# Kernel optimization log

Measured on AMD Instinct MI355X. Metric: run time of the kernel, lower is better.

## Reference

```python
import jax, jax.numpy as jnp
import numpy as np

N_EMBD = 1024
HEAD_SIZE = 128
B, T = 8, 2048


def apply_rope(x):
    # x: (B, T, D); rotate interleaved pairs, matching torch view(B,T,D//2,2)
    b, t, d = x.shape
    freqs = 1.0 / (10000.0 ** (jnp.arange(0, d, 2, dtype=jnp.float32) / d))  # (D//2,)
    angles = jnp.arange(t, dtype=jnp.float32)[:, None] * freqs[None, :]      # (T, D//2)
    cos_a = jnp.cos(angles).astype(x.dtype)
    sin_a = jnp.sin(angles).astype(x.dtype)
    xr = x.reshape(b, t, d // 2, 2)
    x0, x1 = xr[..., 0], xr[..., 1]
    rot = jnp.stack([x0 * cos_a - x1 * sin_a, x0 * sin_a + x1 * cos_a], axis=-1)
    return rot.reshape(b, t, d)


def setup_inputs() -> dict:
    key = jax.random.key(0)
    kx, kq, kk, kv = jax.random.split(key, 4)
    x = jax.random.normal(kx, (B, T, N_EMBD), dtype=jnp.float32)
    scale = 0.02
    Wq = jax.random.normal(kq, (N_EMBD, HEAD_SIZE), dtype=jnp.float32) * scale
    Wk = jax.random.normal(kk, (N_EMBD, HEAD_SIZE), dtype=jnp.float32) * scale
    Wv = jax.random.normal(kv, (N_EMBD, HEAD_SIZE), dtype=jnp.float32) * scale
    return {"x": x, "Wq": Wq, "Wk": Wk, "Wv": Wv}


def reference(x, Wq, Wk, Wv):
    # QKV projections (bias=False)
    q = x @ Wq  # (B, T, H)
    k = x @ Wk
    v = x @ Wv
    q = apply_rope(q)
    k = apply_rope(k)
    d = k.shape[-1]
    wei = jnp.einsum('bqd,bkd->bqk', q, k) * (d ** -0.5)  # (B, T, T)
    causal = jnp.tril(jnp.ones((q.shape[1], q.shape[1]), dtype=bool))
    wei = jnp.where(causal, wei, jnp.finfo(wei.dtype).min)
    wei = jax.nn.softmax(wei, axis=-1)
    out = jnp.einsum('bqk,bkd->bqd', wei, v)  # (B, T, H)
    return out
```

## Files before the change

kernel.cpp:

```cpp
#include <hip/hip_runtime.h>
#include <math.h>

#define BB 8
#define TT 2048
#define EE 1024
#define DD 128

typedef _Float16 f16x8 __attribute__((ext_vector_type(8)));
typedef _Float16 f16x4 __attribute__((ext_vector_type(4)));
typedef float    f32x4 __attribute__((ext_vector_type(4)));
typedef float    f32x16 __attribute__((ext_vector_type(16)));

#define QSCALE 0.12752406f


__global__ __launch_bounds__(256)
void wt_prep_kernel(const float* __restrict__ Wq,
                    const float* __restrict__ Wk,
                    const float* __restrict__ Wv,
                    _Float16* __restrict__ Wb)
{
    int gid = blockIdx.x * 256 + threadIdx.x;
    int kc  = gid / 768;
    int rem = gid - kc * 768;
    int ns  = rem >> 6;
    int ln  = rem & 63;
    int n   = ns * 32 + (ln & 31);
    int k0  = kc * 16 + (ln >> 5) * 8;
    const float* __restrict__ W = (n < 128) ? Wq : (n < 256) ? Wk : Wv;
    int nl = n & 127;
    f16x8 w;
#pragma unroll
    for (int j = 0; j < 8; j++)
        w[j] = (_Float16)W[(size_t)(k0 + j) * DD + nl];
    *(f16x8*)&Wb[(size_t)gid * 8] = w;
}

__global__ __launch_bounds__(256)
void proj_rope_kernel(const float* __restrict__ x,
                      const _Float16* __restrict__ Wb,
                      _Float16* __restrict__ Qb,
                      _Float16* __restrict__ Ka,
                      _Float16* __restrict__ Va)
{
    const int r0   = blockIdx.x * 32;
    const int tid  = threadIdx.x;
    const int wave = tid >> 6;
    const int lane = tid & 63;
    const int half = lane >> 5;
    const int col  = lane & 31;

    __shared__ _Float16 Xb[2][2048];
    __shared__ _Float16 Out[32][136];

    f32x16 acc[3];
#pragma unroll
    for (int s = 0; s < 3; s++) acc[s] = (f32x16)0.f;

    const int sr = tid >> 3;
    const int sc = (tid & 7) * 4;
    const float* __restrict__ xp = &x[(size_t)(r0 + sr) * EE + sc];
    const int w0 = ((sc        >> 4) << 9) + ((sr + 32 * ((sc        >> 3) & 1)) << 3) + (sc & 7);
    const int w1 = (((sc + 32) >> 4) << 9) + ((sr + 32 * (((sc + 32) >> 3) & 1)) << 3) + (sc & 7);

    float4 pa0 = *(const float4*)(xp);
    float4 pa1 = *(const float4*)(xp + 32);
    {
        f16x4 h0 = { (_Float16)pa0.x, (_Float16)pa0.y, (_Float16)pa0.z, (_Float16)pa0.w };
        f16x4 h1 = { (_Float16)pa1.x, (_Float16)pa1.y, (_Float16)pa1.z, (_Float16)pa1.w };
        *(f16x4*)&Xb[0][w0] = h0;
        *(f16x4*)&Xb[0][w1] = h1;
    }
    float4 na0 = *(const float4*)(xp + 64);
    float4 na1 = *(const float4*)(xp + 96);
    float4 nb0 = *(const float4*)(xp + 128);
    float4 nb1 = *(const float4*)(xp + 160);

    for (int it = 0; it < 16; it++) {
        const int buf = it & 1;
        __syncthreads();
        f16x8 a[4], b[12];
#pragma unroll
        for (int kc = 0; kc < 4; kc++)
            a[kc] = *(f16x8*)&Xb[buf][(kc << 9) + lane * 8];
#pragma unroll
        for (int kc = 0; kc < 4; kc++)
#pragma unroll
            for (int s = 0; s < 3; s++)
                b[kc * 3 + s] = *(const f16x8*)&Wb[((size_t)(it * 4 + kc) * 12 + wave * 3 + s) * 512 + lane * 8];
#pragma unroll
        for (int kc = 0; kc < 4; kc++)
#pragma unroll
            for (int s = 0; s < 3; s++)
                acc[s] = __builtin_amdgcn_mfma_f32_32x32x16_f16(a[kc], b[kc * 3 + s], acc[s], 0, 0, 0);
        if (it + 1 < 16) {
            f16x4 h0 = { (_Float16)na0.x, (_Float16)na0.y, (_Float16)na0.z, (_Float16)na0.w };
            f16x4 h1 = { (_Float16)na1.x, (_Float16)na1.y, (_Float16)na1.z, (_Float16)na1.w };
            *(f16x4*)&Xb[buf ^ 1][w0] = h0;
            *(f16x4*)&Xb[buf ^ 1][w1] = h1;
            na0 = nb0; na1 = nb1;
        }
        if (it + 3 < 16) {
            nb0 = *(const float4*)(xp + (it + 3) * 64);
            nb1 = *(const float4*)(xp + (it + 3) * 64 + 32);
        }
    }

    const int bidx = r0 >> 11;
    const int t0   = r0 & (TT - 1);

    for (int p = 0; p < 3; p++) {
        __syncthreads();
#pragma unroll
        for (int s = 0; s < 3; s++) {
            int gs = wave * 3 + s;
            if ((gs >> 2) != p) continue;
            int dcol = (gs & 3) * 32 + col;
            float f = 0.f;
            if (p < 2)
                f = __powf(10000.0f, -(float)(dcol & ~1) * (1.0f / 128.0f));
#pragma unroll
            for (int rg = 0; rg < 16; rg++) {
                int mrow = (rg & 3) + 8 * (rg >> 2) + 4 * half;
                float av = acc[s][rg];
                float res;
                if (p < 2) {
                    float ap = __shfl_xor(av, 1);
                    float sa, ca;
                    __sincosf((float)(t0 + mrow) * f, &sa, &ca);
                    res = av * ca + ap * ((dcol & 1) ? sa : -sa);
                    if (p == 0) res *= QSCALE;
                } else {
                    res = av;
                }
                Out[mrow][dcol] = (_Float16)res;
            }
        }
        __syncthreads();
        if (p < 2) {
            _Float16* __restrict__ dst = (p == 0) ? Qb : Ka;
#pragma unroll
            for (int jj = 0; jj < 2; jj++) {
                int cid = tid + 256 * jj;
                int kc = cid >> 6, ln = cid & 63;
                f16x8 v8 = *(f16x8*)&Out[ln & 31][kc * 16 + (ln >> 5) * 8];
                size_t ga = ((((size_t)bidx * 64 + (t0 >> 5)) * 8 + kc) * 64 + ln) * 8;
                *(f16x8*)&dst[ga] = v8;
            }
        } else {
#pragma unroll
            for (int jj = 0; jj < 2; jj++) {
                int cid = tid + 256 * jj;
                int kcl = cid >> 8, ds = (cid >> 6) & 3, ln = cid & 63;
                f16x8 vv;
#pragma unroll
                for (int e = 0; e < 8; e++)
                    vv[e] = Out[kcl * 16 + (ln >> 5) * 8 + e][ds * 32 + (ln & 31)];
                size_t ga = ((((size_t)bidx * 128 + (t0 >> 4) + kcl) * 4 + ds) * 64 + ln) * 8;
                *(f16x8*)&Va[ga] = vv;
            }
        }
    }
}

__global__ __launch_bounds__(256)
void attn_kernel(const _Float16* __restrict__ Qb,
                 const _Float16* __restrict__ Ka,
                 const _Float16* __restrict__ Va,
                 _Float16* __restrict__ opart,
                 float* __restrict__ mpart,
                 float* __restrict__ lpart)
{
    const int b = blockIdx.y;
    int xt = 15, c = 0;
    {
        int v = 71 - blockIdx.x, s0 = 0;
        for (int j = 0; j < 16; j++) {
            int nc = (j + 2) >> 1;
            if (v < s0 + nc) { xt = j; c = v - s0; break; }
            s0 += nc;
        }
    }
    const int q0 = xt * 128;
    const int nt = 2 * xt + 2;
    const int kt_begin = c * 4;
    const int kt_end   = (kt_begin + 4 < nt) ? (kt_begin + 4) : nt;

    const int tid  = threadIdx.x;
    const int wave = tid >> 6;
    const int lane = tid & 63;
    const int half = lane >> 5;
    const int col  = lane & 31;

    __shared__ _Float16 Kb[8192];
    __shared__ _Float16 Vb[8192];
    __shared__ _Float16 Ps[4][32][72];

    const _Float16* __restrict__ kst = Ka + (size_t)b * 64 * 4096;
    const _Float16* __restrict__ vst = Va + (size_t)b * 128 * 2048;

    const int qg = q0 + wave * 32 + col;
    f16x8 qb[8];
#pragma unroll
    for (int kc = 0; kc < 8; kc++)
        qb[kc] = *(const f16x8*)&Qb[((((size_t)b * 64 + xt * 4 + wave) * 8 + kc) * 64 + lane) * 8];

    f32x16 Of[4];
#pragma unroll
    for (int t = 0; t < 4; t++) Of[t] = (f32x16)0.f;
    float m_ = -1e30f, l_ = 0.f;

    f16x8 kr[4], vr[4];
    {
        const _Float16* kp = kst + (size_t)kt_begin * 8192;
        const _Float16* vp = vst + (size_t)kt_begin * 8192;
#pragma unroll
        for (int i = 0; i < 4; i++) kr[i] = *(const f16x8*)&kp[(tid + 256 * i) * 8];
#pragma unroll
        for (int i = 0; i < 4; i++) vr[i] = *(const f16x8*)&vp[(tid + 256 * i) * 8];
    }

    for (int kt = kt_begin; kt < kt_end; kt++) {
        const int kb0 = kt * 64;
        __syncthreads();
#pragma unroll
        for (int i = 0; i < 4; i++) *(f16x8*)&Kb[(tid + 256 * i) * 8] = kr[i];
#pragma unroll
        for (int i = 0; i < 4; i++) *(f16x8*)&Vb[(tid + 256 * i) * 8] = vr[i];
        __syncthreads();
        if (kt + 1 < kt_end) {
            const _Float16* kp = kst + (size_t)(kt + 1) * 8192;
            const _Float16* vp = vst + (size_t)(kt + 1) * 8192;
#pragma unroll
            for (int i = 0; i < 4; i++) kr[i] = *(const f16x8*)&kp[(tid + 256 * i) * 8];
#pragma unroll
            for (int i = 0; i < 4; i++) vr[i] = *(const f16x8*)&vp[(tid + 256 * i) * 8];
        }

        f32x16 sf[2];
#pragma unroll
        for (int g = 0; g < 2; g++) {
            sf[g] = (f32x16)0.f;
#pragma unroll
            for (int kc = 0; kc < 8; kc++) {
                f16x8 kf = *(f16x8*)&Kb[((g * 8 + kc) * 64 + lane) * 8];
                sf[g] = __builtin_amdgcn_mfma_f32_32x32x16_f16(kf, qb[kc], sf[g], 0, 0, 0);
            }
        }

        const bool diag = (kt >= 2 * xt);
        float mloc = -1e30f;
#pragma unroll
        for (int g = 0; g < 2; g++)
#pragma unroll
            for (int rg = 0; rg < 16; rg++) {
                int key = kb0 + g * 32 + (rg & 3) + 8 * (rg >> 2) + 4 * half;
                float val = sf[g][rg];
                val = (!diag || key <= qg) ? val : -1e30f;
                sf[g][rg] = val;
                mloc = fmaxf(mloc, val);
            }
        mloc = fmaxf(mloc, __shfl_xor(mloc, 32));
        float mnew  = fmaxf(m_, mloc);
        float alpha = __builtin_amdgcn_exp2f(m_ - mnew);
        float ps = 0.f;
#pragma unroll
        for (int g = 0; g < 2; g++) {
#pragma unroll
            for (int rc = 0; rc < 4; rc++) {
                f16x4 p4;
#pragma unroll
                for (int rr = 0; rr < 4; rr++) {
                    float p = __builtin_amdgcn_exp2f(sf[g][4 * rc + rr] - mnew);
                    ps += p;
                    p4[rr] = (_Float16)p;
                }
                *(f16x4*)&Ps[wave][col][g * 32 + 8 * rc + 4 * half] = p4;
            }
        }
        ps += __shfl_xor(ps, 32);
        l_ = l_ * alpha + ps;
        m_ = mnew;
#pragma unroll
        for (int t = 0; t < 4; t++) Of[t] *= alpha;

        f16x8 pb[4];
#pragma unroll
        for (int kc = 0; kc < 4; kc++)
            pb[kc] = *(f16x8*)&Ps[wave][col][kc * 16 + half * 8];
#pragma unroll
        for (int t = 0; t < 4; t++) {
#pragma unroll
            for (int kcl = 0; kcl < 4; kcl++) {
                f16x8 vf = *(f16x8*)&Vb[((kcl * 4 + t) * 64 + lane) * 8];
                Of[t] = __builtin_amdgcn_mfma_f32_32x32x16_f16(vf, pb[kcl], Of[t], 0, 0, 0);
            }
        }
    }

    const int slot = (b * 16 + xt) * 8 + c;
    _Float16* op = opart + ((size_t)slot * 128 + wave * 32 + col) * DD;
#pragma unroll
    for (int t = 0; t < 4; t++) {
#pragma unroll
        for (int rc = 0; rc < 4; rc++) {
            f16x4 o4 = { (_Float16)Of[t][4 * rc + 0], (_Float16)Of[t][4 * rc + 1],
                         (_Float16)Of[t][4 * rc + 2], (_Float16)Of[t][4 * rc + 3] };
            *(f16x4*)&op[t * 32 + 8 * rc + 4 * half] = o4;
        }
    }
    if (half == 0) {
        mpart[slot * 128 + wave * 32 + col] = m_;
        lpart[slot * 128 + wave * 32 + col] = l_;
    }
}

__global__ __launch_bounds__(256)
void combine_kernel(const _Float16* __restrict__ opart,
                    const float* __restrict__ mpart,
                    const float* __restrict__ lpart,
                    float* __restrict__ out)
{
    int gid = blockIdx.x * 256 + threadIdx.x;
    int d   = gid & 127;
    int t   = gid >> 7;
    int b   = t >> 11;
    int tl  = t & (TT - 1);
    int xt  = tl >> 7;
    int rl  = tl & 127;
    int np  = (2 * xt + 5) >> 2;
    int sb  = (b * 16 + xt) * 8;

    float mm = -1e30f;
    for (int j = 0; j < np; j++)
        mm = fmaxf(mm, mpart[(sb + j) * 128 + rl]);
    float acc = 0.f, den = 0.f;
    for (int j = 0; j < np; j++) {
        float w = __builtin_amdgcn_exp2f(mpart[(sb + j) * 128 + rl] - mm);
        den += w * lpart[(sb + j) * 128 + rl];
        acc += w * (float)opart[((size_t)(sb + j) * 128 + rl) * DD + d];
    }
    out[gid] = acc / den;
}

extern "C" void kernel_launch(void* const* d_in, const int* in_sizes, int n_in,
                              void* d_out, int out_size, void* d_ws, size_t ws_size,
                              hipStream_t stream)
{
    const float* x  = (const float*)d_in[0];
    const float* Wq = (const float*)d_in[1];
    const float* Wk = (const float*)d_in[2];
    const float* Wv = (const float*)d_in[3];
    float* out = (float*)d_out;

    const size_t NTOK = (size_t)BB * TT;
    _Float16* Qb = (_Float16*)d_ws;
    _Float16* Ka = Qb + NTOK * DD;
    _Float16* Va = Ka + NTOK * DD;
    _Float16* Wb = Va + NTOK * DD;
    _Float16* opart = Wb + (size_t)384 * EE;
    float* mp = (float*)(opart + (size_t)1024 * 128 * DD);
    float* lp = mp + 1024 * 128;

    wt_prep_kernel<<<dim3(192), dim3(256), 0, stream>>>(Wq, Wk, Wv, Wb);
    proj_rope_kernel<<<dim3(512), dim3(256), 0, stream>>>(x, Wb, Qb, Ka, Va);
    attn_kernel<<<dim3(72, BB), dim3(256), 0, stream>>>(Qb, Ka, Va, opart, mp, lp);
    combine_kernel<<<dim3((int)(NTOK * DD / 256)), dim3(256), 0, stream>>>(opart, mp, lp, out);
}
```

Before: 170.5 us.

## Split projection K-dim across waves, finer attention splits with direct global-to-LDS loads

```diff
diff --git a/kernel.cpp b/kernel.cpp
--- a/kernel.cpp
+++ b/kernel.cpp
@@ -12,6 +12,13 @@
 typedef float    f32x16 __attribute__((ext_vector_type(16)));
 
 #define QSCALE 0.12752406f
+
+__device__ __forceinline__ void gl_lds16(const _Float16* g, _Float16* l)
+{
+    __builtin_amdgcn_global_load_lds(
+        (const __attribute__((address_space(1))) void*)g,
+        (__attribute__((address_space(3))) void*)l, 16, 0, 0);
+}
 
 
 __global__ __launch_bounds__(256)
@@ -36,7 +43,7 @@
     *(f16x8*)&Wb[(size_t)gid * 8] = w;
 }
 
-__global__ __launch_bounds__(256)
+__global__ __launch_bounds__(512, 4)
 void proj_rope_kernel(const float* __restrict__ x,
                       const _Float16* __restrict__ Wb,
                       _Float16* __restrict__ Qb,
@@ -49,61 +56,54 @@
     const int lane = tid & 63;
     const int half = lane >> 5;
     const int col  = lane & 31;
+    const int wave_n = wave & 3;
+    const int wave_k = wave >> 2;
 
     __shared__ _Float16 Xb[2][2048];
+    __shared__ float    Fb[2][32][128];
     __shared__ _Float16 Out[32][136];
 
     f32x16 acc[3];
 #pragma unroll
     for (int s = 0; s < 3; s++) acc[s] = (f32x16)0.f;
 
-    const int sr = tid >> 3;
-    const int sc = (tid & 7) * 4;
+    const int sr = tid >> 4;
+    const int sc = (tid & 15) * 4;
     const float* __restrict__ xp = &x[(size_t)(r0 + sr) * EE + sc];
-    const int w0 = ((sc        >> 4) << 9) + ((sr + 32 * ((sc        >> 3) & 1)) << 3) + (sc & 7);
-    const int w1 = (((sc + 32) >> 4) << 9) + ((sr + 32 * (((sc + 32) >> 3) & 1)) << 3) + (sc & 7);
-
-    float4 pa0 = *(const float4*)(xp);
-    float4 pa1 = *(const float4*)(xp + 32);
+    const int w0 = ((sc >> 4) << 9) + ((sr + 32 * ((sc >> 3) & 1)) << 3) + (sc & 7);
+
+    float4 pa = *(const float4*)(xp);
     {
-        f16x4 h0 = { (_Float16)pa0.x, (_Float16)pa0.y, (_Float16)pa0.z, (_Float16)pa0.w };
-        f16x4 h1 = { (_Float16)pa1.x, (_Float16)pa1.y, (_Float16)pa1.z, (_Float16)pa1.w };
-        *(f16x4*)&Xb[0][w0] = h0;
-        *(f16x4*)&Xb[0][w1] = h1;
-    }
-    float4 na0 = *(const float4*)(xp + 64);
-    float4 na1 = *(const float4*)(xp + 96);
-    float4 nb0 = *(const float4*)(xp + 128);
-    float4 nb1 = *(const float4*)(xp + 160);
+        f16x4 h = { (_Float16)pa.x, (_Float16)pa.y, (_Float16)pa.z, (_Float16)pa.w };
+        *(f16x4*)&Xb[0][w0] = h;
+    }
+    float4 na = *(const float4*)(xp + 64);
+    float4 nb = *(const float4*)(xp + 128);
 
     for (int it = 0; it < 16; it++) {
         const int buf = it & 1;
         __syncthreads();
-        f16x8 a[4], b[12];
-#pragma unroll
-        for (int kc = 0; kc < 4; kc++)
-            a[kc] = *(f16x8*)&Xb[buf][(kc << 9) + lane * 8];
-#pragma unroll
-        for (int kc = 0; kc < 4; kc++)
+        f16x8 a[2], b[6];
+#pragma unroll
+        for (int kl = 0; kl < 2; kl++)
+            a[kl] = *(f16x8*)&Xb[buf][((wave_k * 2 + kl) << 9) + lane * 8];
+#pragma unroll
+        for (int kl = 0; kl < 2; kl++)
 #pragma unroll
             for (int s = 0; s < 3; s++)
-                b[kc * 3 + s] = *(const f16x8*)&Wb[((size_t)(it * 4 + kc) * 12 + wave * 3 + s) * 512 + lane * 8];
-#pragma unroll
-        for (int kc = 0; kc < 4; kc++)
+                b[kl * 3 + s] = *(const f16x8*)&Wb[((size_t)(it * 4 + wave_k * 2 + kl) * 12 + wave_n * 3 + s) * 512 + lane * 8];
+#pragma unroll
+        for (int kl = 0; kl < 2; kl++)
 #pragma unroll
             for (int s = 0; s < 3; s++)
-                acc[s] = __builtin_amdgcn_mfma_f32_32x32x16_f16(a[kc], b[kc * 3 + s], acc[s], 0, 0, 0);
+                acc[s] = __builtin_amdgcn_mfma_f32_32x32x16_f16(a[kl], b[kl * 3 + s], acc[s], 0, 0, 0);
         if (it + 1 < 16) {
-            f16x4 h0 = { (_Float16)na0.x, (_Float16)na0.y, (_Float16)na0.z, (_Float16)na0.w };
-            f16x4 h1 = { (_Float16)na1.x, (_Float16)na1.y, (_Float16)na1.z, (_Float16)na1.w };
-            *(f16x4*)&Xb[buf ^ 1][w0] = h0;
-            *(f16x4*)&Xb[buf ^ 1][w1] = h1;
-            na0 = nb0; na1 = nb1;
-        }
-        if (it + 3 < 16) {
-            nb0 = *(const float4*)(xp + (it + 3) * 64);
-            nb1 = *(const float4*)(xp + (it + 3) * 64 + 32);
-        }
+            f16x4 h = { (_Float16)na.x, (_Float16)na.y, (_Float16)na.z, (_Float16)na.w };
+            *(f16x4*)&Xb[buf ^ 1][w0] = h;
+            na = nb;
+        }
+        if (it + 3 < 16)
+            nb = *(const float4*)(xp + (it + 3) * 64);
     }
 
     const int bidx = r0 >> 11;
@@ -113,57 +113,61 @@
         __syncthreads();
 #pragma unroll
         for (int s = 0; s < 3; s++) {
-            int gs = wave * 3 + s;
+            int gs = wave_n * 3 + s;
             if ((gs >> 2) != p) continue;
             int dcol = (gs & 3) * 32 + col;
-            float f = 0.f;
-            if (p < 2)
-                f = __powf(10000.0f, -(float)(dcol & ~1) * (1.0f / 128.0f));
 #pragma unroll
             for (int rg = 0; rg < 16; rg++) {
                 int mrow = (rg & 3) + 8 * (rg >> 2) + 4 * half;
-                float av = acc[s][rg];
-                float res;
-                if (p < 2) {
-                    float ap = __shfl_xor(av, 1);
-                    float sa, ca;
-                    __sincosf((float)(t0 + mrow) * f, &sa, &ca);
-                    res = av * ca + ap * ((dcol & 1) ? sa : -sa);
-                    if (p == 0) res *= QSCALE;
-                } else {
-                    res = av;
-                }
-                Out[mrow][dcol] = (_Float16)res;
+                Fb[wave_k][mrow][dcol] = acc[s][rg];
+            }
+        }
+        __syncthreads();
+        if (p < 2) {
+#pragma unroll
+            for (int q = 0; q < 4; q++) {
+                int pid = tid * 4 + q;
+                int row = pid >> 6;
+                int cp  = pid & 63;
+                float v0 = Fb[0][row][2 * cp]     + Fb[1][row][2 * cp];
+                float v1 = Fb[0][row][2 * cp + 1] + Fb[1][row][2 * cp + 1];
+                float f  = __powf(10000.0f, -(float)(2 * cp) * (1.0f / 128.0f));
+                float sa, ca;
+                __sincosf((float)(t0 + row) * f, &sa, &ca);
+                float e0 = v0 * ca - v1 * sa;
+                float e1 = v0 * sa + v1 * ca;
+                if (p == 0) { e0 *= QSCALE; e1 *= QSCALE; }
+                Out[row][2 * cp]     = (_Float16)e0;
+                Out[row][2 * cp + 1] = (_Float16)e1;
+            }
+        } else {
+#pragma unroll
+            for (int q = 0; q < 8; q++) {
+                int eid = tid * 8 + q;
+                int row = eid >> 7, cc = eid & 127;
+                Out[row][cc] = (_Float16)(Fb[0][row][cc] + Fb[1][row][cc]);
             }
         }
         __syncthreads();
         if (p < 2) {
             _Float16* __restrict__ dst = (p == 0) ? Qb : Ka;
-#pragma unroll
-            for (int jj = 0; jj < 2; jj++) {
-                int cid = tid + 256 * jj;
-                int kc = cid >> 6, ln = cid & 63;
-                f16x8 v8 = *(f16x8*)&Out[ln & 31][kc * 16 + (ln >> 5) * 8];
-                size_t ga = ((((size_t)bidx * 64 + (t0 >> 5)) * 8 + kc) * 64 + ln) * 8;
-                *(f16x8*)&dst[ga] = v8;
-            }
+            int kc = tid >> 6, ln = tid & 63;
+            f16x8 v8 = *(f16x8*)&Out[ln & 31][kc * 16 + (ln >> 5) * 8];
+            size_t ga = ((((size_t)bidx * 64 + (t0 >> 5)) * 8 + kc) * 64 + ln) * 8;
+            *(f16x8*)&dst[ga] = v8;
         } else {
-#pragma unroll
-            for (int jj = 0; jj < 2; jj++) {
-                int cid = tid + 256 * jj;
-                int kcl = cid >> 8, ds = (cid >> 6) & 3, ln = cid & 63;
-                f16x8 vv;
-#pragma unroll
-                for (int e = 0; e < 8; e++)
-                    vv[e] = Out[kcl * 16 + (ln >> 5) * 8 + e][ds * 32 + (ln & 31)];
-                size_t ga = ((((size_t)bidx * 128 + (t0 >> 4) + kcl) * 4 + ds) * 64 + ln) * 8;
-                *(f16x8*)&Va[ga] = vv;
-            }
-        }
-    }
-}
-
-__global__ __launch_bounds__(256)
+            int kcl = tid >> 8, ds = (tid >> 6) & 3, ln = tid & 63;
+            f16x8 vv;
+#pragma unroll
+            for (int e = 0; e < 8; e++)
+                vv[e] = Out[kcl * 16 + (ln >> 5) * 8 + e][ds * 32 + (ln & 31)];
+            size_t ga = ((((size_t)bidx * 128 + (t0 >> 4) + kcl) * 4 + ds) * 64 + ln) * 8;
+            *(f16x8*)&Va[ga] = vv;
+        }
+    }
+}
+
+__global__ __launch_bounds__(256, 3)
 void attn_kernel(const _Float16* __restrict__ Qb,
                  const _Float16* __restrict__ Ka,
                  const _Float16* __restrict__ Va,
@@ -174,17 +178,14 @@
     const int b = blockIdx.y;
     int xt = 15, c = 0;
     {
-        int v = 71 - blockIdx.x, s0 = 0;
+        int v = blockIdx.x, s0 = 0;
         for (int j = 0; j < 16; j++) {
-            int nc = (j + 2) >> 1;
-            if (v < s0 + nc) { xt = j; c = v - s0; break; }
-            s0 += nc;
-        }
-    }
-    const int q0 = xt * 128;
-    const int nt = 2 * xt + 2;
-    const int kt_begin = c * 4;
-    const int kt_end   = (kt_begin + 4 < nt) ? (kt_begin + 4) : nt;
+            if (v < s0 + j + 1) { xt = j; c = v - s0; break; }
+            s0 += j + 1;
+        }
+    }
+    const int q0  = xt * 128;
+    const int kt0 = 2 * c;
 
     const int tid  = threadIdx.x;
     const int wave = tid >> 6;
@@ -210,32 +211,22 @@
     for (int t = 0; t < 4; t++) Of[t] = (f32x16)0.f;
     float m_ = -1e30f, l_ = 0.f;
 
-    f16x8 kr[4], vr[4];
     {
-        const _Float16* kp = kst + (size_t)kt_begin * 8192;
-        const _Float16* vp = vst + (size_t)kt_begin * 8192;
-#pragma unroll
-        for (int i = 0; i < 4; i++) kr[i] = *(const f16x8*)&kp[(tid + 256 * i) * 8];
-#pragma unroll
-        for (int i = 0; i < 4; i++) vr[i] = *(const f16x8*)&vp[(tid + 256 * i) * 8];
-    }
-
-    for (int kt = kt_begin; kt < kt_end; kt++) {
+        const _Float16* kp = kst + (size_t)kt0 * 8192 + (size_t)tid * 8;
+        const _Float16* vp = vst + (size_t)kt0 * 8192 + (size_t)tid * 8;
+#pragma unroll
+        for (int i = 0; i < 4; i++) {
+            gl_lds16(kp + (size_t)i * 2048, &Kb[(wave * 64 + i * 256) * 8]);
+            gl_lds16(vp + (size_t)i * 2048, &Vb[(wave * 64 + i * 256) * 8]);
+        }
+    }
+
+#pragma unroll
+    for (int tt = 0; tt < 2; tt++) {
+        const int kt  = kt0 + tt;
         const int kb0 = kt * 64;
-        __syncthreads();
-#pragma unroll
-        for (int i = 0; i < 4; i++) *(f16x8*)&Kb[(tid + 256 * i) * 8] = kr[i];
-#pragma unroll
-        for (int i = 0; i < 4; i++) *(f16x8*)&Vb[(tid + 256 * i) * 8] = vr[i];
-        __syncthreads();
-        if (kt + 1 < kt_end) {
-            const _Float16* kp = kst + (size_t)(kt + 1) * 8192;
-            const _Float16* vp = vst + (size_t)(kt + 1) * 8192;
-#pragma unroll
-            for (int i = 0; i < 4; i++) kr[i] = *(const f16x8*)&kp[(tid + 256 * i) * 8];
-#pragma unroll
-            for (int i = 0; i < 4; i++) vr[i] = *(const f16x8*)&vp[(tid + 256 * i) * 8];
-        }
+        asm volatile("s_waitcnt vmcnt(0)" ::: "memory");
+        __syncthreads();
 
         f32x16 sf[2];
 #pragma unroll
@@ -296,9 +287,20 @@
                 Of[t] = __builtin_amdgcn_mfma_f32_32x32x16_f16(vf, pb[kcl], Of[t], 0, 0, 0);
             }
         }
-    }
-
-    const int slot = (b * 16 + xt) * 8 + c;
+
+        if (tt == 0) {
+            __syncthreads();
+            const _Float16* kp = kst + (size_t)(kt0 + 1) * 8192 + (size_t)tid * 8;
+            const _Float16* vp = vst + (size_t)(kt0 + 1) * 8192 + (size_t)tid * 8;
+#pragma unroll
+            for (int i = 0; i < 4; i++) {
+                gl_lds16(kp + (size_t)i * 2048, &Kb[(wave * 64 + i * 256) * 8]);
+                gl_lds16(vp + (size_t)i * 2048, &Vb[(wave * 64 + i * 256) * 8]);
+            }
+        }
+    }
+
+    const int slot = (b * 16 + xt) * 16 + c;
     _Float16* op = opart + ((size_t)slot * 128 + wave * 32 + col) * DD;
 #pragma unroll
     for (int t = 0; t < 4; t++) {
@@ -328,8 +330,8 @@
     int tl  = t & (TT - 1);
     int xt  = tl >> 7;
     int rl  = tl & 127;
-    int np  = (2 * xt + 5) >> 2;
-    int sb  = (b * 16 + xt) * 8;
+    int np  = xt + 1;
+    int sb  = (b * 16 + xt) * 16;
 
     float mm = -1e30f;
     for (int j = 0; j < np; j++)
@@ -359,11 +361,11 @@
     _Float16* Va = Ka + NTOK * DD;
     _Float16* Wb = Va + NTOK * DD;
     _Float16* opart = Wb + (size_t)384 * EE;
-    float* mp = (float*)(opart + (size_t)1024 * 128 * DD);
-    float* lp = mp + 1024 * 128;
+    float* mp = (float*)(opart + (size_t)2048 * 128 * DD);
+    float* lp = mp + 2048 * 128;
 
     wt_prep_kernel<<<dim3(192), dim3(256), 0, stream>>>(Wq, Wk, Wv, Wb);
-    proj_rope_kernel<<<dim3(512), dim3(256), 0, stream>>>(x, Wb, Qb, Ka, Va);
-    attn_kernel<<<dim3(72, BB), dim3(256), 0, stream>>>(Qb, Ka, Va, opart, mp, lp);
+    proj_rope_kernel<<<dim3(512), dim3(512), 0, stream>>>(x, Wb, Qb, Ka, Va);
+    attn_kernel<<<dim3(136, BB), dim3(256), 0, stream>>>(Qb, Ka, Va, opart, mp, lp);
     combine_kernel<<<dim3((int)(NTOK * DD / 256)), dim3(256), 0, stream>>>(opart, mp, lp, out);
 }
```

Measured after the change: 193.9 us. +13.7%, slower.
